# Performance work log

Measured on AMD Instinct MI355X. Metric: run time of the kernel, lower is better.

The kernel has to match this reference:

```python
import jax, jax.numpy as jnp
import numpy as np

N_FALSE_NEG = 64
TEMPERATURE = 0.1
NORMALIZE = True

B, T, D = 32, 512, 512
M = 4096


def setup_inputs() -> dict:
    key = jax.random.key(0)
    k1, k2, k3 = jax.random.split(key, 3)
    input_predicted = jax.random.normal(k1, (B, T, D), dtype=jnp.float32)
    input_encoded = jax.random.normal(k2, (B, T, D), dtype=jnp.float32)
    rows = jax.random.randint(k3, (M,), 0, B)
    cols = jax.random.randint(jax.random.fold_in(k3, 1), (M,), 0, T)
    mask_ids = jnp.stack([rows, cols], axis=1).astype(jnp.int64)
    return {"input_predicted": input_predicted, "input_encoded": input_encoded, "mask_ids": mask_ids}


def _l2norm(x, eps=1e-12):
    # matches F.normalize(p=2, dim=-1)
    n = jnp.sqrt(jnp.sum(x * x, axis=-1, keepdims=True))
    return x / jnp.maximum(n, eps)


def reference(input_predicted, input_encoded, mask_ids):
    m = mask_ids.shape[0]
    rows, cols = mask_ids[:, 0], mask_ids[:, 1]
    enc = input_encoded[rows, cols]      # [M, D] encoded at masked positions
    preds = input_predicted[rows, cols]  # [M, D]

    # negatives_from_same_seq_only=False branch:
    # candidates = arange(0, M-1); idx_pos = i; torch.randint(0, M-2) -> [0, M-3]
    r = jax.random.randint(jax.random.key(42), (m, N_FALSE_NEG), 0, m - 2)  # [M, K]
    i = jnp.arange(m)[:, None]
    sel = r + (r >= i).astype(r.dtype)   # skip the positive index
    negatives = enc[sel]                 # [M, K, D]

    candidates = jnp.concatenate([enc[:, None, :], negatives], axis=1)  # [M, K+1, D]
    if NORMALIZE:
        candidates = _l2norm(candidates)
        preds = _l2norm(preds)

    sim = jnp.einsum('md,mcd->mc', preds, candidates) / TEMPERATURE  # [M, K+1]
    # cross entropy with target class 0
    lse = jax.nn.logsumexp(sim, axis=-1)
    loss = jnp.mean(lse - sim[:, 0])
    acc = jnp.mean((jnp.argmax(sim, axis=-1) == 0).astype(jnp.float32))
    return loss, acc
```

## Files before the change

### kernel.cpp

```cpp
#include <hip/hip_runtime.h>
#include <stdint.h>

#define T_DIM 512
#define D_DIM 512
#define M_ROWS 4096
#define NNEG 64
#define INV_TEMP 10.0f
#define SPAN 4094u
#define MULT 1024u

typedef short v8s __attribute__((ext_vector_type(8)));
typedef float v4f __attribute__((ext_vector_type(4)));

struct U2 { uint32_t a, b; };

__host__ __device__ constexpr uint32_t rotl32(uint32_t x, uint32_t r) {
  return (x << r) | (x >> (32u - r));
}

__host__ __device__ constexpr U2 tf2x32(uint32_t k0, uint32_t k1,
                                        uint32_t c0, uint32_t c1) {
  uint32_t ks0 = k0, ks1 = k1, ks2 = k0 ^ k1 ^ 0x1BD11BDAu;
  uint32_t x0 = c0 + ks0, x1 = c1 + ks1;
  x0 += x1; x1 = rotl32(x1, 13); x1 ^= x0;
  x0 += x1; x1 = rotl32(x1, 15); x1 ^= x0;
  x0 += x1; x1 = rotl32(x1, 26); x1 ^= x0;
  x0 += x1; x1 = rotl32(x1, 6);  x1 ^= x0;
  x0 += ks1; x1 += ks2 + 1u;
  x0 += x1; x1 = rotl32(x1, 17); x1 ^= x0;
  x0 += x1; x1 = rotl32(x1, 29); x1 ^= x0;
  x0 += x1; x1 = rotl32(x1, 16); x1 ^= x0;
  x0 += x1; x1 = rotl32(x1, 24); x1 ^= x0;
  x0 += ks2; x1 += ks0 + 2u;
  x0 += x1; x1 = rotl32(x1, 13); x1 ^= x0;
  x0 += x1; x1 = rotl32(x1, 15); x1 ^= x0;
  x0 += x1; x1 = rotl32(x1, 26); x1 ^= x0;
  x0 += x1; x1 = rotl32(x1, 6);  x1 ^= x0;
  x0 += ks0; x1 += ks1 + 3u;
  x0 += x1; x1 = rotl32(x1, 17); x1 ^= x0;
  x0 += x1; x1 = rotl32(x1, 29); x1 ^= x0;
  x0 += x1; x1 = rotl32(x1, 16); x1 ^= x0;
  x0 += x1; x1 = rotl32(x1, 24); x1 ^= x0;
  x0 += ks1; x1 += ks2 + 4u;
  x0 += x1; x1 = rotl32(x1, 13); x1 ^= x0;
  x0 += x1; x1 = rotl32(x1, 15); x1 ^= x0;
  x0 += x1; x1 = rotl32(x1, 26); x1 ^= x0;
  x0 += x1; x1 = rotl32(x1, 6);  x1 ^= x0;
  x0 += ks2; x1 += ks0 + 5u;
  return U2{x0, x1};
}

constexpr U2 KHI = tf2x32(0u, 42u, 0u, 0u);
constexpr U2 KLO = tf2x32(0u, 42u, 0u, 1u);

__device__ inline uint32_t sel_index(uint32_t m, uint32_t j) {
  uint32_t pos = m * 64u + j;
  U2 h = tf2x32(KHI.a, KHI.b, 0u, pos);
  U2 l = tf2x32(KLO.a, KLO.b, 0u, pos);
  uint32_t hi = h.a ^ h.b;
  uint32_t lo = l.a ^ l.b;
  uint32_t r = ((hi % SPAN) * MULT + (lo % SPAN)) % SPAN;
  return r + (r >= m ? 1u : 0u);
}

__device__ inline uint32_t pack_bf2(float lo, float hi) {
  uint32_t ul = __float_as_uint(lo); ul += 0x7fffu + ((ul >> 16) & 1u);
  uint32_t uh = __float_as_uint(hi); uh += 0x7fffu + ((uh >> 16) & 1u);
  return (ul >> 16) | (uh & 0xffff0000u);
}
__device__ inline float bflo(int v) { return __uint_as_float(((uint32_t)v) << 16); }
__device__ inline float bfhi(int v) { return __uint_as_float(((uint32_t)v) & 0xffff0000u); }

__global__ __launch_bounds__(256) void k_norm_enc(
    const float* __restrict__ enc, const int* __restrict__ ids,
    int4* __restrict__ nenc) {
  int lane = threadIdx.x & 63;
  int wave = threadIdx.x >> 6;
  int m = blockIdx.x * 4 + wave;

  int2 rc = ((const int2*)ids)[m];
  size_t base = ((size_t)rc.x * T_DIM + rc.y) * D_DIM;
  const float4* ep = (const float4*)(enc + base);
  float4 e0 = ep[2 * lane], e1 = ep[2 * lane + 1];

  float se = e0.x*e0.x + e0.y*e0.y + e0.z*e0.z + e0.w*e0.w
           + e1.x*e1.x + e1.y*e1.y + e1.z*e1.z + e1.w*e1.w;
  #pragma unroll
  for (int off = 1; off < 64; off <<= 1) se += __shfl_xor(se, off, 64);
  float inv_e = 1.0f / fmaxf(sqrtf(se), 1e-12f);

  int4 eq;
  eq.x = pack_bf2(e0.x * inv_e, e0.y * inv_e);
  eq.y = pack_bf2(e0.z * inv_e, e0.w * inv_e);
  eq.z = pack_bf2(e1.x * inv_e, e1.y * inv_e);
  eq.w = pack_bf2(e1.z * inv_e, e1.w * inv_e);
  nenc[m * 64 + lane] = eq;
}

__global__ __launch_bounds__(256) void k_contrast(
    const float* __restrict__ pred, const int* __restrict__ ids,
    const int4* __restrict__ nenc, float2* __restrict__ partials) {
  int lane = threadIdx.x & 63;
  int wave = threadIdx.x >> 6;
  int m = blockIdx.x * 4 + wave;
  int col = lane & 15;
  int quad = lane >> 4;

  __shared__ int sel_lds[4][64];
  __shared__ int4 p_lds[4][64];
  __shared__ float2 wred[4];

  int2 rc = ((const int2*)ids)[m];
  size_t base = ((size_t)rc.x * T_DIM + rc.y) * D_DIM;
  const float4* pp = (const float4*)(pred + base);
  float4 p0 = pp[2 * lane], p1 = pp[2 * lane + 1];
  float sp = p0.x*p0.x + p0.y*p0.y + p0.z*p0.z + p0.w*p0.w
           + p1.x*p1.x + p1.y*p1.y + p1.z*p1.z + p1.w*p1.w;
  #pragma unroll
  for (int off = 1; off < 64; off <<= 1) sp += __shfl_xor(sp, off, 64);
  float inv_p = 1.0f / fmaxf(sqrtf(sp), 1e-12f);
  float pn0 = p0.x*inv_p, pn1 = p0.y*inv_p, pn2 = p0.z*inv_p, pn3 = p0.w*inv_p;
  float pn4 = p1.x*inv_p, pn5 = p1.y*inv_p, pn6 = p1.z*inv_p, pn7 = p1.w*inv_p;

  int4 pq;
  pq.x = pack_bf2(pn0, pn1); pq.y = pack_bf2(pn2, pn3);
  pq.z = pack_bf2(pn4, pn5); pq.w = pack_bf2(pn6, pn7);
  p_lds[wave][lane] = pq;
  sel_lds[wave][lane] = (int)sel_index((uint32_t)m, (uint32_t)lane);

  int4 eq = nenc[m * 64 + lane];
  float dp = pn0 * bflo(eq.x);
  dp = fmaf(pn1, bfhi(eq.x), dp);
  dp = fmaf(pn2, bflo(eq.y), dp);
  dp = fmaf(pn3, bfhi(eq.y), dp);
  dp = fmaf(pn4, bflo(eq.z), dp);
  dp = fmaf(pn5, bfhi(eq.z), dp);
  dp = fmaf(pn6, bflo(eq.w), dp);
  dp = fmaf(pn7, bfhi(eq.w), dp);
  #pragma unroll
  for (int off = 1; off < 64; off <<= 1) dp += __shfl_xor(dp, off, 64);
  float s0 = dp * INV_TEMP;

  const int4* aptr[4];
  #pragma unroll
  for (int c = 0; c < 4; ++c) {
    int sel = sel_lds[wave][16 * c + col];
    aptr[c] = nenc + (size_t)sel * 64;
  }

  v4f acc0 = {0,0,0,0}, acc1 = {0,0,0,0}, acc2 = {0,0,0,0}, acc3 = {0,0,0,0};
  const char* pbase = (const char*)&p_lds[wave][0];

  #pragma unroll 4
  for (int t = 0; t < 16; ++t) {
    v8s b = *(const v8s*)(pbase + 64 * t + 16 * quad);
    int idx = 4 * t + quad;
    union { int4 i; v8s s; } a0, a1, a2, a3;
    a0.i = aptr[0][idx]; a1.i = aptr[1][idx];
    a2.i = aptr[2][idx]; a3.i = aptr[3][idx];
    acc0 = __builtin_amdgcn_mfma_f32_16x16x32_bf16(a0.s, b, acc0, 0, 0, 0);
    acc1 = __builtin_amdgcn_mfma_f32_16x16x32_bf16(a1.s, b, acc1, 0, 0, 0);
    acc2 = __builtin_amdgcn_mfma_f32_16x16x32_bf16(a2.s, b, acc2, 0, 0, 0);
    acc3 = __builtin_amdgcn_mfma_f32_16x16x32_bf16(a3.s, b, acc3, 0, 0, 0);
  }

  float se = 0.0f, maxneg = -1e30f;
  #pragma unroll
  for (int r = 0; r < 4; ++r) {
    float s_0 = acc0[r] * INV_TEMP, s_1 = acc1[r] * INV_TEMP;
    float s_2 = acc2[r] * INV_TEMP, s_3 = acc3[r] * INV_TEMP;
    maxneg = fmaxf(fmaxf(fmaxf(maxneg, s_0), fmaxf(s_1, s_2)), s_3);
    se += __expf(s_0) + __expf(s_1) + __expf(s_2) + __expf(s_3);
  }
  se += __shfl_xor(se, 16, 64);
  se += __shfl_xor(se, 32, 64);
  maxneg = fmaxf(maxneg, __shfl_xor(maxneg, 16, 64));
  maxneg = fmaxf(maxneg, __shfl_xor(maxneg, 32, 64));

  if (lane == 0) {
    float lse = logf(se + __expf(s0));
    wred[wave] = make_float2(lse - s0, (s0 >= maxneg) ? 1.0f : 0.0f);
  }
  __syncthreads();
  if (threadIdx.x == 0) {
    float l = 0.0f, a = 0.0f;
    #pragma unroll
    for (int w = 0; w < 4; ++w) { l += wred[w].x; a += wred[w].y; }
    partials[blockIdx.x] = make_float2(l, a);
  }
}

__global__ __launch_bounds__(256) void k_finalize(
    const float2* __restrict__ partials, float* __restrict__ out) {
  int t = threadIdx.x;
  float l = 0.0f, a = 0.0f;
  #pragma unroll
  for (int i = 0; i < 4; ++i) {
    float2 v = partials[t + 256 * i];
    l += v.x; a += v.y;
  }
  #pragma unroll
  for (int off = 1; off < 64; off <<= 1) {
    l += __shfl_xor(l, off, 64);
    a += __shfl_xor(a, off, 64);
  }
  __shared__ float2 wred[4];
  if ((t & 63) == 0) wred[t >> 6] = make_float2(l, a);
  __syncthreads();
  if (t == 0) {
    out[0] = (wred[0].x + wred[1].x + wred[2].x + wred[3].x) * (1.0f / M_ROWS);
    out[1] = (wred[0].y + wred[1].y + wred[2].y + wred[3].y) * (1.0f / M_ROWS);
  }
}

extern "C" void kernel_launch(void* const* d_in, const int* in_sizes, int n_in,
                              void* d_out, int out_size, void* d_ws, size_t ws_size,
                              hipStream_t stream) {
  const float* pred = (const float*)d_in[0];
  const float* enc  = (const float*)d_in[1];
  const int*   ids  = (const int*)d_in[2];
  float* out = (float*)d_out;

  int4* nenc = (int4*)d_ws;
  float2* partials = (float2*)(nenc + (size_t)M_ROWS * 64);

  k_norm_enc<<<M_ROWS / 4, 256, 0, stream>>>(enc, ids, nenc);
  k_contrast<<<M_ROWS / 4, 256, 0, stream>>>(pred, ids, nenc, partials);
  k_finalize<<<1, 256, 0, stream>>>(partials, out);
}
```

Measured before the change: 123.8 us.

## Store normalized encodings as FP8 and replace MFMA with per-lane dot products

The normalized encoded rows are now stored as FP8 (e4m3 via cvt_pk_fp8) instead of bf16, halving the workspace footprint and the gather traffic for the 64 negatives per row. The MFMA bf16 matmul is replaced with a scalar FMA loop over negatives: each lane dequantizes 8 values per negative, then a wave-wide shuffle reduction follows. This cuts memory bytes but adds many shuffle reductions (6 per negative), and FP8 precision may shift logits enough to change the loss or the accuracy comparison.

```diff
diff --git a/kernel.cpp b/kernel.cpp
--- a/kernel.cpp
+++ b/kernel.cpp
@@ -9,8 +9,7 @@
 #define SPAN 4094u
 #define MULT 1024u
 
-typedef short v8s __attribute__((ext_vector_type(8)));
-typedef float v4f __attribute__((ext_vector_type(4)));
+typedef float v2f __attribute__((ext_vector_type(2)));
 
 struct U2 { uint32_t a, b; };
 
@@ -63,17 +62,9 @@
   return r + (r >= m ? 1u : 0u);
 }
 
-__device__ inline uint32_t pack_bf2(float lo, float hi) {
-  uint32_t ul = __float_as_uint(lo); ul += 0x7fffu + ((ul >> 16) & 1u);
-  uint32_t uh = __float_as_uint(hi); uh += 0x7fffu + ((uh >> 16) & 1u);
-  return (ul >> 16) | (uh & 0xffff0000u);
-}
-__device__ inline float bflo(int v) { return __uint_as_float(((uint32_t)v) << 16); }
-__device__ inline float bfhi(int v) { return __uint_as_float(((uint32_t)v) & 0xffff0000u); }
-
 __global__ __launch_bounds__(256) void k_norm_enc(
     const float* __restrict__ enc, const int* __restrict__ ids,
-    int4* __restrict__ nenc) {
+    int2* __restrict__ nenc) {
   int lane = threadIdx.x & 63;
   int wave = threadIdx.x >> 6;
   int m = blockIdx.x * 4 + wave;
@@ -89,26 +80,36 @@
   for (int off = 1; off < 64; off <<= 1) se += __shfl_xor(se, off, 64);
   float inv_e = 1.0f / fmaxf(sqrtf(se), 1e-12f);
 
-  int4 eq;
-  eq.x = pack_bf2(e0.x * inv_e, e0.y * inv_e);
-  eq.y = pack_bf2(e0.z * inv_e, e0.w * inv_e);
-  eq.z = pack_bf2(e1.x * inv_e, e1.y * inv_e);
-  eq.w = pack_bf2(e1.z * inv_e, e1.w * inv_e);
-  nenc[m * 64 + lane] = eq;
+  int w0 = __builtin_amdgcn_cvt_pk_fp8_f32(e0.x * inv_e, e0.y * inv_e, 0, false);
+  w0     = __builtin_amdgcn_cvt_pk_fp8_f32(e0.z * inv_e, e0.w * inv_e, w0, true);
+  int w1 = __builtin_amdgcn_cvt_pk_fp8_f32(e1.x * inv_e, e1.y * inv_e, 0, false);
+  w1     = __builtin_amdgcn_cvt_pk_fp8_f32(e1.z * inv_e, e1.w * inv_e, w1, true);
+  nenc[m * 64 + lane] = make_int2(w0, w1);
+}
+
+__device__ inline float dot8_fp8(int2 q, const float* pn) {
+  v2f a = __builtin_amdgcn_cvt_pk_f32_fp8(q.x, false);
+  float d = pn[0] * a.x;
+  d = fmaf(pn[1], a.y, d);
+  a = __builtin_amdgcn_cvt_pk_f32_fp8(q.x, true);
+  d = fmaf(pn[2], a.x, d); d = fmaf(pn[3], a.y, d);
+  a = __builtin_amdgcn_cvt_pk_f32_fp8(q.y, false);
+  d = fmaf(pn[4], a.x, d); d = fmaf(pn[5], a.y, d);
+  a = __builtin_amdgcn_cvt_pk_f32_fp8(q.y, true);
+  d = fmaf(pn[6], a.x, d); d = fmaf(pn[7], a.y, d);
+  return d;
 }
 
 __global__ __launch_bounds__(256) void k_contrast(
     const float* __restrict__ pred, const int* __restrict__ ids,
-    const int4* __restrict__ nenc, float2* __restrict__ partials) {
+    const int2* __restrict__ nenc, float2* __restrict__ partials) {
   int lane = threadIdx.x & 63;
   int wave = threadIdx.x >> 6;
   int m = blockIdx.x * 4 + wave;
-  int col = lane & 15;
-  int quad = lane >> 4;
 
   __shared__ int sel_lds[4][64];
-  __shared__ int4 p_lds[4][64];
   __shared__ float2 wred[4];
+  sel_lds[wave][lane] = (int)sel_index((uint32_t)m, (uint32_t)lane);
 
   int2 rc = ((const int2*)ids)[m];
   size_t base = ((size_t)rc.x * T_DIM + rc.y) * D_DIM;
@@ -119,66 +120,44 @@
   #pragma unroll
   for (int off = 1; off < 64; off <<= 1) sp += __shfl_xor(sp, off, 64);
   float inv_p = 1.0f / fmaxf(sqrtf(sp), 1e-12f);
-  float pn0 = p0.x*inv_p, pn1 = p0.y*inv_p, pn2 = p0.z*inv_p, pn3 = p0.w*inv_p;
-  float pn4 = p1.x*inv_p, pn5 = p1.y*inv_p, pn6 = p1.z*inv_p, pn7 = p1.w*inv_p;
-
-  int4 pq;
-  pq.x = pack_bf2(pn0, pn1); pq.y = pack_bf2(pn2, pn3);
-  pq.z = pack_bf2(pn4, pn5); pq.w = pack_bf2(pn6, pn7);
-  p_lds[wave][lane] = pq;
-  sel_lds[wave][lane] = (int)sel_index((uint32_t)m, (uint32_t)lane);
-
-  int4 eq = nenc[m * 64 + lane];
-  float dp = pn0 * bflo(eq.x);
-  dp = fmaf(pn1, bfhi(eq.x), dp);
-  dp = fmaf(pn2, bflo(eq.y), dp);
-  dp = fmaf(pn3, bfhi(eq.y), dp);
-  dp = fmaf(pn4, bflo(eq.z), dp);
-  dp = fmaf(pn5, bfhi(eq.z), dp);
-  dp = fmaf(pn6, bflo(eq.w), dp);
-  dp = fmaf(pn7, bfhi(eq.w), dp);
+
+  float pn[8];
+  pn[0] = p0.x*inv_p; pn[1] = p0.y*inv_p; pn[2] = p0.z*inv_p; pn[3] = p0.w*inv_p;
+  pn[4] = p1.x*inv_p; pn[5] = p1.y*inv_p; pn[6] = p1.z*inv_p; pn[7] = p1.w*inv_p;
+
+  float dp = dot8_fp8(nenc[m * 64 + lane], pn);
   #pragma unroll
   for (int off = 1; off < 64; off <<= 1) dp += __shfl_xor(dp, off, 64);
   float s0 = dp * INV_TEMP;
 
-  const int4* aptr[4];
-  #pragma unroll
-  for (int c = 0; c < 4; ++c) {
-    int sel = sel_lds[wave][16 * c + col];
-    aptr[c] = nenc + (size_t)sel * 64;
-  }
-
-  v4f acc0 = {0,0,0,0}, acc1 = {0,0,0,0}, acc2 = {0,0,0,0}, acc3 = {0,0,0,0};
-  const char* pbase = (const char*)&p_lds[wave][0];
-
-  #pragma unroll 4
-  for (int t = 0; t < 16; ++t) {
-    v8s b = *(const v8s*)(pbase + 64 * t + 16 * quad);
-    int idx = 4 * t + quad;
-    union { int4 i; v8s s; } a0, a1, a2, a3;
-    a0.i = aptr[0][idx]; a1.i = aptr[1][idx];
-    a2.i = aptr[2][idx]; a3.i = aptr[3][idx];
-    acc0 = __builtin_amdgcn_mfma_f32_16x16x32_bf16(a0.s, b, acc0, 0, 0, 0);
-    acc1 = __builtin_amdgcn_mfma_f32_16x16x32_bf16(a1.s, b, acc1, 0, 0, 0);
-    acc2 = __builtin_amdgcn_mfma_f32_16x16x32_bf16(a2.s, b, acc2, 0, 0, 0);
-    acc3 = __builtin_amdgcn_mfma_f32_16x16x32_bf16(a3.s, b, acc3, 0, 0, 0);
-  }
-
-  float se = 0.0f, maxneg = -1e30f;
-  #pragma unroll
-  for (int r = 0; r < 4; ++r) {
-    float s_0 = acc0[r] * INV_TEMP, s_1 = acc1[r] * INV_TEMP;
-    float s_2 = acc2[r] * INV_TEMP, s_3 = acc3[r] * INV_TEMP;
+  float sumexp = __expf(s0);
+  float maxneg = -1e30f;
+
+  for (int jj = 0; jj < NNEG; jj += 4) {
+    int4 s4 = *((const int4*)&sel_lds[wave][jj]);
+    int2 q0 = nenc[(size_t)s4.x * 64 + lane];
+    int2 q1 = nenc[(size_t)s4.y * 64 + lane];
+    int2 q2 = nenc[(size_t)s4.z * 64 + lane];
+    int2 q3 = nenc[(size_t)s4.w * 64 + lane];
+    float d0 = dot8_fp8(q0, pn);
+    float d1 = dot8_fp8(q1, pn);
+    float d2 = dot8_fp8(q2, pn);
+    float d3 = dot8_fp8(q3, pn);
+    #pragma unroll
+    for (int off = 1; off < 64; off <<= 1) {
+      d0 += __shfl_xor(d0, off, 64);
+      d1 += __shfl_xor(d1, off, 64);
+      d2 += __shfl_xor(d2, off, 64);
+      d3 += __shfl_xor(d3, off, 64);
+    }
+    float s_0 = d0 * INV_TEMP, s_1 = d1 * INV_TEMP;
+    float s_2 = d2 * INV_TEMP, s_3 = d3 * INV_TEMP;
     maxneg = fmaxf(fmaxf(fmaxf(maxneg, s_0), fmaxf(s_1, s_2)), s_3);
-    se += __expf(s_0) + __expf(s_1) + __expf(s_2) + __expf(s_3);
-  }
-  se += __shfl_xor(se, 16, 64);
-  se += __shfl_xor(se, 32, 64);
-  maxneg = fmaxf(maxneg, __shfl_xor(maxneg, 16, 64));
-  maxneg = fmaxf(maxneg, __shfl_xor(maxneg, 32, 64));
+    sumexp += __expf(s_0) + __expf(s_1) + __expf(s_2) + __expf(s_3);
+  }
 
   if (lane == 0) {
-    float lse = logf(se + __expf(s0));
+    float lse = logf(sumexp);
     wred[wave] = make_float2(lse - s0, (s0 >= maxneg) ? 1.0f : 0.0f);
   }
   __syncthreads();
@@ -221,7 +200,7 @@
   const int*   ids  = (const int*)d_in[2];
   float* out = (float*)d_out;
 
-  int4* nenc = (int4*)d_ws;
+  int2* nenc = (int2*)d_ws;
   float2* partials = (float2*)(nenc + (size_t)M_ROWS * 64);
 
   k_norm_enc<<<M_ROWS / 4, 256, 0, stream>>>(enc, ids, nenc);
```

After: 115.1 us. 7.0% less time.
